# Performance work log

Measured on AMD Instinct MI355X. Metric: run time of the kernel, lower is better.

## Reference

```python
import jax, jax.numpy as jnp
import numpy as np


def _chamfer_sq(points, gts):
    # points: [B,N,3], gts: [B,M,3]
    pn = jnp.sum(points * points, axis=-1)              # [B,N]
    gn = jnp.sum(gts * gts, axis=-1)                    # [B,M]
    cross = jnp.einsum('bnd,bmd->bnm', points, gts)     # [B,N,M]
    d = pn[:, :, None] + gn[:, None, :] - 2.0 * cross   # [B,N,M]
    d = jnp.maximum(d, 0.0)
    p2g = jnp.min(d, axis=2)                            # [B,N] squared NN dist
    g2p = jnp.min(d, axis=1)                            # [B,M]
    return p2g, g2p


def setup_inputs() -> dict:
    key = jax.random.key(0)
    k1, k2 = jax.random.split(key)
    B, N, M = 8, 4096, 4096
    points = jax.random.normal(k1, (B, N, 3), dtype=jnp.float32)
    gts = jax.random.normal(k2, (B, M, 3), dtype=jnp.float32)
    return {"points": points, "gts": gts}


def reference(points, gts):
    p2g_sq, g2p_sq = _chamfer_sq(points, gts)
    p2g = jnp.sqrt(jnp.mean(p2g_sq, axis=1))   # [B]
    g2p = jnp.sqrt(jnp.mean(g2p_sq, axis=1))   # [B]
    loss = (p2g + g2p) / 2.0
    return (jnp.mean(loss), jnp.mean(p2g), jnp.mean(g2p))
```

## Files before the change

### kernel.cpp

```cpp
#include <hip/hip_runtime.h>
#include <math.h>

#define NPTS 4096
#define NB   8
#define QCB  512
#define RCB  512
#define NQC  (NPTS / QCB)
#define NRC  (NPTS / RCB)
#define NRT  (RCB / 32)

typedef _Float16 h8     __attribute__((ext_vector_type(8)));
typedef float    f32x16 __attribute__((ext_vector_type(16)));

__device__ __forceinline__ void split2(float v, _Float16& h, _Float16& l) {
    h = (_Float16)v;
    l = (_Float16)(v - (float)h);
}

__global__ __launch_bounds__(1024, 2) void chamfer_mfma32(
    const float* __restrict__ P, const float* __restrict__ G,
    float* __restrict__ qpart,
    float* __restrict__ rpart,
    int* __restrict__ counter)
{
    __shared__ __align__(16) unsigned char smem[73728];
    h8*    Bfr  = (h8*)smem;
    int*   rbuf = (int*)(smem + 16384);
    float* qbufall = (float*)smem;

    const int b    = blockIdx.y;
    const int qc   = blockIdx.x >> 3;
    const int rc   = blockIdx.x & 7;
    const int tid  = threadIdx.x;
    const int w    = tid >> 6;
    const int lane = tid & 63;
    const int col  = lane & 31;
    const int kg   = lane >> 5;

    if (blockIdx.x == 0 && blockIdx.y == 0 && tid == 0) *counter = 0;

    const float* __restrict__ Pb = P + (size_t)b * NPTS * 3;
    const float* __restrict__ Gb = G + (size_t)b * NPTS * 3;

    const _Float16 one = (_Float16)1.f, zr = (_Float16)0.f;

    if (tid < 512) rbuf[tid] = 0x7f7fffff;
    for (int e = tid; e < NRT * 64; e += 1024) {
        const int el   = e & 63;
        const int ecol = el & 31, ekg = el >> 5;
        const int ref  = rc * RCB + (e >> 6) * 32 + ecol;
        const float gx = Gb[3 * ref], gy = Gb[3 * ref + 1], gz = Gb[3 * ref + 2];
        const float gn = fmaf(gx, gx, fmaf(gy, gy, gz * gz));
        _Float16 xh, xl, yh, yl, zh, zl, nh, nl;
        split2(gx, xh, xl); split2(gy, yh, yl); split2(gz, zh, zl); split2(gn, nh, nl);
        Bfr[e] = ekg ? (h8){one, nh, xl, yl, zl, zr, nl, zr}
                     : (h8){xh, yh, zh, one, nh, xh, yh, zh};
    }

    const int q0 = qc * QCB + w * 32 + col;
    const float px = Pb[3 * q0], py = Pb[3 * q0 + 1], pz = Pb[3 * q0 + 2];
    const float m2x = -2.f * px, m2y = -2.f * py, m2z = -2.f * pz;
    const float pn = fmaf(px, px, fmaf(py, py, pz * pz));
    _Float16 axh, axl, ayh, ayl, azh, azl, aph, apl;
    split2(m2x, axh, axl); split2(m2y, ayh, ayl); split2(m2z, azh, azl); split2(pn, aph, apl);
    const h8 afr = kg ? (h8){apl, zr, axh, ayh, azh, aph, one, zr}
                      : (h8){axh, ayh, azh, aph, one, axl, ayl, azl};

    f32x16 qacc;
#pragma unroll
    for (int j = 0; j < 16; ++j) qacc[j] = 3.4e38f;

    __syncthreads();

    const f32x16 cz = (f32x16){0.f,0.f,0.f,0.f,0.f,0.f,0.f,0.f,
                               0.f,0.f,0.f,0.f,0.f,0.f,0.f,0.f};
#pragma unroll 4
    for (int rt = 0; rt < NRT; ++rt) {
        const h8 bfr = Bfr[rt * 64 + lane];
        f32x16 d = __builtin_amdgcn_mfma_f32_32x32x16_f16(afr, bfr, cz, 0, 0, 0);
#pragma unroll
        for (int j = 0; j < 16; ++j) qacc[j] = fminf(qacc[j], d[j]);
        float t0 = fminf(fminf(d[0],  d[1]),  d[2]);
        float t1 = fminf(fminf(d[3],  d[4]),  d[5]);
        float t2 = fminf(fminf(d[6],  d[7]),  d[8]);
        float t3 = fminf(fminf(d[9],  d[10]), d[11]);
        float t4 = fminf(fminf(d[12], d[13]), d[14]);
        float v  = fminf(fminf(fminf(t0, t1), t2), fminf(fminf(t3, t4), d[15]));
        v = fmaxf(v, 0.f);
        atomicMin(&rbuf[rt * 32 + col], __float_as_int(v));
    }

    __syncthreads();
    if (tid < RCB)
        rpart[((size_t)b * NQC + qc) * NPTS + rc * RCB + tid] = __int_as_float(rbuf[tid]);
    __syncthreads();

    float* qw = qbufall + w * 1152;
#pragma unroll
    for (int j = 0; j < 16; ++j) {
        const int row = (j & 3) + 8 * (j >> 2) + 4 * kg;
        qw[row * 36 + col] = qacc[j];
    }
    __syncthreads();
    if (lane < 32) {
        const float4* qr = (const float4*)(qw + col * 36);
        float4 v = qr[0];
#pragma unroll
        for (int k = 1; k < 8; ++k) {
            float4 u = qr[k];
            v.x = fminf(v.x, u.x); v.y = fminf(v.y, u.y);
            v.z = fminf(v.z, u.z); v.w = fminf(v.w, u.w);
        }
        const float rowmin = fminf(fminf(v.x, v.y), fminf(v.z, v.w));
        qpart[((size_t)b * NRC + rc) * NPTS + qc * QCB + w * 32 + col] = rowmin;
    }
}

__global__ __launch_bounds__(256) void chamfer_reduce2(
    const float* __restrict__ qpart, const float* __restrict__ rpart,
    float* __restrict__ sums, int* __restrict__ counter,
    float* __restrict__ out)
{
    const int path = blockIdx.x >> 5;
    const int b    = (blockIdx.x >> 2) & 7;
    const int sp   = blockIdx.x & 3;
    const float* __restrict__ base = (path ? rpart : qpart) + (size_t)b * 8 * NPTS;

    float sum = 0.f;
#pragma unroll
    for (int i = 0; i < 4; ++i) {
        const int q = sp * 1024 + i * 256 + threadIdx.x;
        float mn = base[q];
#pragma unroll
        for (int c = 1; c < 8; ++c) mn = fminf(mn, base[(size_t)c * NPTS + q]);
        sum += fmaxf(mn, 0.f);
    }

    __shared__ float red[256];
    __shared__ int amLast;
    red[threadIdx.x] = sum;
    __syncthreads();
    if (threadIdx.x < 128) red[threadIdx.x] += red[threadIdx.x + 128];
    __syncthreads();
    if (threadIdx.x < 64) {
        float v = red[threadIdx.x] + red[threadIdx.x + 64];
#pragma unroll
        for (int off = 32; off > 0; off >>= 1) v += __shfl_down(v, off, 64);
        if (threadIdx.x == 0) {
            sums[blockIdx.x] = v;
            __threadfence();
            amLast = (atomicAdd(counter, 1) == 63);
        }
    }
    __syncthreads();

    if (amLast) {
        __shared__ float r16[16];
        if (threadIdx.x < 16) {
            float s = 0.f;
#pragma unroll
            for (int k = 0; k < 4; ++k)
                s += *(volatile const float*)&sums[threadIdx.x * 4 + k];
            r16[threadIdx.x] = sqrtf(s / (float)NPTS);
        }
        __syncthreads();
        if (threadIdx.x == 0) {
            float p2g = 0.f, g2p = 0.f;
#pragma unroll
            for (int bb = 0; bb < NB; ++bb) { p2g += r16[bb]; g2p += r16[NB + bb]; }
            p2g *= (1.0f / NB);
            g2p *= (1.0f / NB);
            out[0] = 0.5f * (p2g + g2p);
            out[1] = p2g;
            out[2] = g2p;
            *counter = 0;
        }
    }
}

extern "C" void kernel_launch(void* const* d_in, const int* in_sizes, int n_in,
                              void* d_out, int out_size, void* d_ws, size_t ws_size,
                              hipStream_t stream) {
    const float* points = (const float*)d_in[0];
    const float* gts    = (const float*)d_in[1];
    float* out = (float*)d_out;

    float* qpart = (float*)d_ws;
    float* rpart = qpart + (size_t)NB * NRC * NPTS;
    float* sums  = rpart + (size_t)NB * NQC * NPTS;
    int*   counter = (int*)(sums + 64);

    dim3 grid1(NQC * NRC, NB);
    chamfer_mfma32<<<grid1, 1024, 0, stream>>>(points, gts, qpart, rpart, counter);

    chamfer_reduce2<<<dim3(64), 256, 0, stream>>>(qpart, rpart, sums, counter, out);
}
```

Measured before the change: 20.51 us.

## Replace per-chunk partial buffers with global atomicMin reductions and an init kernel

The main kernel now folds its per-reference and per-query chunk minima straight into global [B,N] buffers with unsigned atomicMin. This works because the values are clamped to be non-negative, so their float bits order correctly as unsigned integers. The 8-way partial arrays go away, and the final reduce kernel reads only one value per point instead of taking a min over 8 partials. In exchange, a separate init kernel launch is needed to fill the buffers with the max value and reset the counter, and writes become contended global atomics. The change also fully unrolls the reference-tile loop, trims the transpose padding, and drops one block barrier, since each wave only reads its own LDS region.

```diff
diff --git a/kernel.cpp b/kernel.cpp
--- a/kernel.cpp
+++ b/kernel.cpp
@@ -5,9 +5,7 @@
 #define NB   8
 #define QCB  512
 #define RCB  512
-#define NQC  (NPTS / QCB)
-#define NRC  (NPTS / RCB)
-#define NRT  (RCB / 32)
+#define NRT  16
 
 typedef _Float16 h8     __attribute__((ext_vector_type(8)));
 typedef float    f32x16 __attribute__((ext_vector_type(16)));
@@ -17,16 +15,21 @@
     l = (_Float16)(v - (float)h);
 }
 
+__global__ __launch_bounds__(1024) void chamfer_init(unsigned* __restrict__ buf,
+                                                     int* __restrict__ counter) {
+    buf[blockIdx.x * 1024 + threadIdx.x] = 0xFFFFFFFFu;
+    if (blockIdx.x == 0 && threadIdx.x == 0) *counter = 0;
+}
+
 __global__ __launch_bounds__(1024, 2) void chamfer_mfma32(
     const float* __restrict__ P, const float* __restrict__ G,
-    float* __restrict__ qpart,
-    float* __restrict__ rpart,
-    int* __restrict__ counter)
+    unsigned* __restrict__ qmin,
+    unsigned* __restrict__ rmin)
 {
-    __shared__ __align__(16) unsigned char smem[73728];
+    __shared__ __align__(16) unsigned char smem[69632];
     h8*    Bfr  = (h8*)smem;
     int*   rbuf = (int*)(smem + 16384);
-    float* qbufall = (float*)smem;
+    float* qtr  = (float*)smem;
 
     const int b    = blockIdx.y;
     const int qc   = blockIdx.x >> 3;
@@ -37,24 +40,22 @@
     const int col  = lane & 31;
     const int kg   = lane >> 5;
 
-    if (blockIdx.x == 0 && blockIdx.y == 0 && tid == 0) *counter = 0;
-
     const float* __restrict__ Pb = P + (size_t)b * NPTS * 3;
     const float* __restrict__ Gb = G + (size_t)b * NPTS * 3;
 
     const _Float16 one = (_Float16)1.f, zr = (_Float16)0.f;
 
-    if (tid < 512) rbuf[tid] = 0x7f7fffff;
-    for (int e = tid; e < NRT * 64; e += 1024) {
-        const int el   = e & 63;
+    if (tid < RCB) rbuf[tid] = 0x7f7fffff;
+    {
+        const int el   = tid & 63;
         const int ecol = el & 31, ekg = el >> 5;
-        const int ref  = rc * RCB + (e >> 6) * 32 + ecol;
+        const int ref  = rc * RCB + (tid >> 6) * 32 + ecol;
         const float gx = Gb[3 * ref], gy = Gb[3 * ref + 1], gz = Gb[3 * ref + 2];
         const float gn = fmaf(gx, gx, fmaf(gy, gy, gz * gz));
         _Float16 xh, xl, yh, yl, zh, zl, nh, nl;
         split2(gx, xh, xl); split2(gy, yh, yl); split2(gz, zh, zl); split2(gn, nh, nl);
-        Bfr[e] = ekg ? (h8){one, nh, xl, yl, zl, zr, nl, zr}
-                     : (h8){xh, yh, zh, one, nh, xh, yh, zh};
+        Bfr[tid] = ekg ? (h8){one, nh, xl, yl, zl, zr, nl, zr}
+                       : (h8){xh, yh, zh, one, nh, xh, yh, zh};
     }
 
     const int q0 = qc * QCB + w * 32 + col;
@@ -74,7 +75,7 @@
 
     const f32x16 cz = (f32x16){0.f,0.f,0.f,0.f,0.f,0.f,0.f,0.f,
                                0.f,0.f,0.f,0.f,0.f,0.f,0.f,0.f};
-#pragma unroll 4
+#pragma unroll
     for (int rt = 0; rt < NRT; ++rt) {
         const h8 bfr = Bfr[rt * 64 + lane];
         f32x16 d = __builtin_amdgcn_mfma_f32_32x32x16_f16(afr, bfr, cz, 0, 0, 0);
@@ -92,53 +93,45 @@
 
     __syncthreads();
     if (tid < RCB)
-        rpart[((size_t)b * NQC + qc) * NPTS + rc * RCB + tid] = __int_as_float(rbuf[tid]);
+        atomicMin(&rmin[(size_t)b * NPTS + rc * RCB + tid], (unsigned)rbuf[tid]);
     __syncthreads();
 
-    float* qw = qbufall + w * 1152;
+    float* qw = qtr + w * (32 * 34);
 #pragma unroll
     for (int j = 0; j < 16; ++j) {
         const int row = (j & 3) + 8 * (j >> 2) + 4 * kg;
-        qw[row * 36 + col] = qacc[j];
+        qw[row * 34 + col] = qacc[j];
     }
-    __syncthreads();
     if (lane < 32) {
-        const float4* qr = (const float4*)(qw + col * 36);
-        float4 v = qr[0];
+        const float2* qr = (const float2*)(qw + lane * 34);
+        float m = 3.4e38f;
 #pragma unroll
-        for (int k = 1; k < 8; ++k) {
-            float4 u = qr[k];
-            v.x = fminf(v.x, u.x); v.y = fminf(v.y, u.y);
-            v.z = fminf(v.z, u.z); v.w = fminf(v.w, u.w);
+        for (int k = 0; k < 16; ++k) {
+            float2 u = qr[k];
+            m = fminf(m, fminf(u.x, u.y));
         }
-        const float rowmin = fminf(fminf(v.x, v.y), fminf(v.z, v.w));
-        qpart[((size_t)b * NRC + rc) * NPTS + qc * QCB + w * 32 + col] = rowmin;
+        atomicMin(&qmin[(size_t)b * NPTS + qc * QCB + w * 32 + lane],
+                  __float_as_uint(fmaxf(m, 0.f)));
     }
 }
 
 __global__ __launch_bounds__(256) void chamfer_reduce2(
-    const float* __restrict__ qpart, const float* __restrict__ rpart,
-    float* __restrict__ sums, int* __restrict__ counter,
-    float* __restrict__ out)
+    const unsigned* __restrict__ qmin, const unsigned* __restrict__ rmin,
+    float* __restrict__ sums, int* __restrict__ counter, float* __restrict__ out)
 {
-    const int path = blockIdx.x >> 5;
-    const int b    = (blockIdx.x >> 2) & 7;
-    const int sp   = blockIdx.x & 3;
-    const float* __restrict__ base = (path ? rpart : qpart) + (size_t)b * 8 * NPTS;
+    const int t  = blockIdx.x >> 2;
+    const int sp = blockIdx.x & 3;
+    const unsigned* __restrict__ base =
+        (t >= 8) ? rmin + (size_t)(t - 8) * NPTS : qmin + (size_t)t * NPTS;
 
-    float sum = 0.f;
+    float s = 0.f;
 #pragma unroll
-    for (int i = 0; i < 4; ++i) {
-        const int q = sp * 1024 + i * 256 + threadIdx.x;
-        float mn = base[q];
-#pragma unroll
-        for (int c = 1; c < 8; ++c) mn = fminf(mn, base[(size_t)c * NPTS + q]);
-        sum += fmaxf(mn, 0.f);
-    }
+    for (int i = 0; i < 4; ++i)
+        s += __uint_as_float(base[sp * 1024 + i * 256 + threadIdx.x]);
 
     __shared__ float red[256];
     __shared__ int amLast;
-    red[threadIdx.x] = sum;
+    red[threadIdx.x] = s;
     __syncthreads();
     if (threadIdx.x < 128) red[threadIdx.x] += red[threadIdx.x + 128];
     __syncthreads();
@@ -157,11 +150,11 @@
     if (amLast) {
         __shared__ float r16[16];
         if (threadIdx.x < 16) {
-            float s = 0.f;
+            float acc = 0.f;
 #pragma unroll
             for (int k = 0; k < 4; ++k)
-                s += *(volatile const float*)&sums[threadIdx.x * 4 + k];
-            r16[threadIdx.x] = sqrtf(s / (float)NPTS);
+                acc += *(volatile const float*)&sums[threadIdx.x * 4 + k];
+            r16[threadIdx.x] = sqrtf(acc / (float)NPTS);
         }
         __syncthreads();
         if (threadIdx.x == 0) {
@@ -185,13 +178,15 @@
     const float* gts    = (const float*)d_in[1];
     float* out = (float*)d_out;
 
-    float* qpart = (float*)d_ws;
-    float* rpart = qpart + (size_t)NB * NRC * NPTS;
-    float* sums  = rpart + (size_t)NB * NQC * NPTS;
-    int*   counter = (int*)(sums + 64);
+    unsigned* qmin = (unsigned*)d_ws;
+    unsigned* rmin = qmin + (size_t)NB * NPTS;
+    float*    sums = (float*)(rmin + (size_t)NB * NPTS);
+    int*      counter = (int*)(sums + 64);
 
-    dim3 grid1(NQC * NRC, NB);
-    chamfer_mfma32<<<grid1, 1024, 0, stream>>>(points, gts, qpart, rpart, counter);
+    chamfer_init<<<dim3(64), 1024, 0, stream>>>(qmin, counter);
 
-    chamfer_reduce2<<<dim3(64), 256, 0, stream>>>(qpart, rpart, sums, counter, out);
+    dim3 grid1(64, NB);
+    chamfer_mfma32<<<grid1, 1024, 0, stream>>>(points, gts, qmin, rmin);
+
+    chamfer_reduce2<<<dim3(64), 256, 0, stream>>>(qmin, rmin, sums, counter, out);
 }
```

Measured after the change: 23.61 us (median of 2 runs). 15.1% more time.

## Compute both chamfer directions as separate row-min passes instead of LDS atomics

Applied to the files above, without the earlier changes.

The per-tile column minimum via LDS atomicMin is dropped. The pairwise distances are instead computed twice, once per direction (a grid z-dimension swaps points and gts), and only row-min reduction is used. Each wave now holds four query tiles in registers and reuses each B fragment across four MFMAs, with 256-thread blocks over 1024-reference chunks. This removes atomic contention and the LDS column reduction, but doubles the MFMA work and the number of blocks.

```diff
diff --git a/kernel.cpp b/kernel.cpp
--- a/kernel.cpp
+++ b/kernel.cpp
@@ -4,52 +4,54 @@
 #define NPTS 4096
 #define NB   8
 #define QCB  512
-#define RCB  512
+#define RCB  1024
 #define NQC  (NPTS / QCB)
 #define NRC  (NPTS / RCB)
-#define NRT  (RCB / 32)
 
 typedef _Float16 h8     __attribute__((ext_vector_type(8)));
 typedef float    f32x16 __attribute__((ext_vector_type(16)));
+
+#define FOREACH_T(OP) OP(0) OP(1) OP(2) OP(3)
 
 __device__ __forceinline__ void split2(float v, _Float16& h, _Float16& l) {
     h = (_Float16)v;
     l = (_Float16)(v - (float)h);
 }
 
-__global__ __launch_bounds__(1024, 2) void chamfer_mfma32(
+__global__ __launch_bounds__(256, 2) void chamfer_mfma32(
     const float* __restrict__ P, const float* __restrict__ G,
     float* __restrict__ qpart,
     float* __restrict__ rpart,
     int* __restrict__ counter)
 {
-    __shared__ __align__(16) unsigned char smem[73728];
-    h8*    Bfr  = (h8*)smem;
-    int*   rbuf = (int*)(smem + 16384);
-    float* qbufall = (float*)smem;
+    __shared__ __align__(16) unsigned char smem[32768];
+    h8*    Bfr = (h8*)smem;
+    float* qtr = (float*)smem;
 
-    const int b    = blockIdx.y;
-    const int qc   = blockIdx.x >> 3;
-    const int rc   = blockIdx.x & 7;
-    const int tid  = threadIdx.x;
+    const int dir = blockIdx.z;
+    const int b   = blockIdx.y;
+    const int qc  = blockIdx.x >> 2;
+    const int rc  = blockIdx.x & 3;
+    const int tid = threadIdx.x;
     const int w    = tid >> 6;
     const int lane = tid & 63;
     const int col  = lane & 31;
     const int kg   = lane >> 5;
 
-    if (blockIdx.x == 0 && blockIdx.y == 0 && tid == 0) *counter = 0;
+    if (blockIdx.x == 0 && b == 0 && dir == 0 && tid == 0) *counter = 0;
 
-    const float* __restrict__ Pb = P + (size_t)b * NPTS * 3;
-    const float* __restrict__ Gb = G + (size_t)b * NPTS * 3;
+    const float* __restrict__ Qb = (dir ? G : P) + (size_t)b * NPTS * 3;
+    const float* __restrict__ Rb = (dir ? P : G) + (size_t)b * NPTS * 3;
 
     const _Float16 one = (_Float16)1.f, zr = (_Float16)0.f;
 
-    if (tid < 512) rbuf[tid] = 0x7f7fffff;
-    for (int e = tid; e < NRT * 64; e += 1024) {
+#pragma unroll
+    for (int i = 0; i < 8; ++i) {
+        const int e    = tid + i * 256;
         const int el   = e & 63;
         const int ecol = el & 31, ekg = el >> 5;
         const int ref  = rc * RCB + (e >> 6) * 32 + ecol;
-        const float gx = Gb[3 * ref], gy = Gb[3 * ref + 1], gz = Gb[3 * ref + 2];
+        const float gx = Rb[3 * ref], gy = Rb[3 * ref + 1], gz = Rb[3 * ref + 2];
         const float gn = fmaf(gx, gx, fmaf(gy, gy, gz * gz));
         _Float16 xh, xl, yh, yl, zh, zl, nh, nl;
         split2(gx, xh, xl); split2(gy, yh, yl); split2(gz, zh, zl); split2(gn, nh, nl);
@@ -57,74 +59,73 @@
                      : (h8){xh, yh, zh, one, nh, xh, yh, zh};
     }
 
-    const int q0 = qc * QCB + w * 32 + col;
-    const float px = Pb[3 * q0], py = Pb[3 * q0 + 1], pz = Pb[3 * q0 + 2];
-    const float m2x = -2.f * px, m2y = -2.f * py, m2z = -2.f * pz;
-    const float pn = fmaf(px, px, fmaf(py, py, pz * pz));
-    _Float16 axh, axl, ayh, ayl, azh, azl, aph, apl;
-    split2(m2x, axh, axl); split2(m2y, ayh, ayl); split2(m2z, azh, azl); split2(pn, aph, apl);
-    const h8 afr = kg ? (h8){apl, zr, axh, ayh, azh, aph, one, zr}
-                      : (h8){axh, ayh, azh, aph, one, axl, ayl, azl};
-
-    f32x16 qacc;
-#pragma unroll
-    for (int j = 0; j < 16; ++j) qacc[j] = 3.4e38f;
+#define DECLT(t) h8 afr##t; f32x16 qa##t;
+    FOREACH_T(DECLT)
+#undef DECLT
+#define MKA(t) { \
+        const int q0 = qc * QCB + w * 128 + (t) * 32 + col;                   \
+        const float px = Qb[3 * q0], py = Qb[3 * q0 + 1], pz = Qb[3 * q0 + 2];\
+        const float m2x = -2.f * px, m2y = -2.f * py, m2z = -2.f * pz;        \
+        const float pn = fmaf(px, px, fmaf(py, py, pz * pz));                 \
+        _Float16 xh, xl, yh, yl, zh, zl, ph, pl;                              \
+        split2(m2x, xh, xl); split2(m2y, yh, yl); split2(m2z, zh, zl);        \
+        split2(pn, ph, pl);                                                   \
+        afr##t = kg ? (h8){pl, zr, xh, yh, zh, ph, one, zr}                   \
+                    : (h8){xh, yh, zh, ph, one, xl, yl, zl};                  \
+        _Pragma("unroll")                                                     \
+        for (int j = 0; j < 16; ++j) qa##t[j] = 3.4e38f; }
+    FOREACH_T(MKA)
+#undef MKA
 
     __syncthreads();
 
     const f32x16 cz = (f32x16){0.f,0.f,0.f,0.f,0.f,0.f,0.f,0.f,
                                0.f,0.f,0.f,0.f,0.f,0.f,0.f,0.f};
-#pragma unroll 4
-    for (int rt = 0; rt < NRT; ++rt) {
+#pragma unroll 2
+    for (int rt = 0; rt < 32; ++rt) {
         const h8 bfr = Bfr[rt * 64 + lane];
-        f32x16 d = __builtin_amdgcn_mfma_f32_32x32x16_f16(afr, bfr, cz, 0, 0, 0);
-#pragma unroll
-        for (int j = 0; j < 16; ++j) qacc[j] = fminf(qacc[j], d[j]);
-        float t0 = fminf(fminf(d[0],  d[1]),  d[2]);
-        float t1 = fminf(fminf(d[3],  d[4]),  d[5]);
-        float t2 = fminf(fminf(d[6],  d[7]),  d[8]);
-        float t3 = fminf(fminf(d[9],  d[10]), d[11]);
-        float t4 = fminf(fminf(d[12], d[13]), d[14]);
-        float v  = fminf(fminf(fminf(t0, t1), t2), fminf(fminf(t3, t4), d[15]));
-        v = fmaxf(v, 0.f);
-        atomicMin(&rbuf[rt * 32 + col], __float_as_int(v));
+#define DOT(t) { \
+        f32x16 d = __builtin_amdgcn_mfma_f32_32x32x16_f16(afr##t, bfr, cz, 0, 0, 0); \
+        _Pragma("unroll")                                                     \
+        for (int j = 0; j < 16; ++j) qa##t[j] = fminf(qa##t[j], d[j]); }
+        FOREACH_T(DOT)
+#undef DOT
     }
 
     __syncthreads();
-    if (tid < RCB)
-        rpart[((size_t)b * NQC + qc) * NPTS + rc * RCB + tid] = __int_as_float(rbuf[tid]);
-    __syncthreads();
 
-    float* qw = qbufall + w * 1152;
-#pragma unroll
-    for (int j = 0; j < 16; ++j) {
-        const int row = (j & 3) + 8 * (j >> 2) + 4 * kg;
-        qw[row * 36 + col] = qacc[j];
-    }
-    __syncthreads();
-    if (lane < 32) {
-        const float4* qr = (const float4*)(qw + col * 36);
-        float4 v = qr[0];
-#pragma unroll
-        for (int k = 1; k < 8; ++k) {
-            float4 u = qr[k];
-            v.x = fminf(v.x, u.x); v.y = fminf(v.y, u.y);
-            v.z = fminf(v.z, u.z); v.w = fminf(v.w, u.w);
-        }
-        const float rowmin = fminf(fminf(v.x, v.y), fminf(v.z, v.w));
-        qpart[((size_t)b * NRC + rc) * NPTS + qc * QCB + w * 32 + col] = rowmin;
-    }
+    float* qw = qtr + w * 1088;
+    float* outb = (dir ? rpart : qpart)
+                + ((size_t)b * NRC + rc) * NPTS + qc * QCB + w * 128;
+#define EPI(t) { \
+        _Pragma("unroll")                                                     \
+        for (int j = 0; j < 16; ++j) {                                        \
+            const int row = (j & 3) + 8 * (j >> 2) + 4 * kg;                  \
+            qw[row * 34 + col] = qa##t[j];                                    \
+        }                                                                     \
+        if (lane < 32) {                                                      \
+            const float2* qr = (const float2*)(qw + lane * 34);               \
+            float m = 3.4e38f;                                                \
+            _Pragma("unroll")                                                 \
+            for (int k = 0; k < 16; ++k) {                                    \
+                float2 u = qr[k];                                             \
+                m = fminf(m, fminf(u.x, u.y));                                \
+            }                                                                 \
+            outb[(t) * 32 + lane] = fmaxf(m, 0.f);                            \
+        } }
+    FOREACH_T(EPI)
+#undef EPI
 }
 
 __global__ __launch_bounds__(256) void chamfer_reduce2(
     const float* __restrict__ qpart, const float* __restrict__ rpart,
-    float* __restrict__ sums, int* __restrict__ counter,
-    float* __restrict__ out)
+    float* __restrict__ sums, int* __restrict__ counter, float* __restrict__ out)
 {
-    const int path = blockIdx.x >> 5;
-    const int b    = (blockIdx.x >> 2) & 7;
-    const int sp   = blockIdx.x & 3;
-    const float* __restrict__ base = (path ? rpart : qpart) + (size_t)b * 8 * NPTS;
+    const int t  = blockIdx.x >> 2;
+    const int sp = blockIdx.x & 3;
+    const float* __restrict__ base =
+        (t >= 8 ? rpart + (size_t)(t - 8) * NRC * NPTS
+                : qpart + (size_t)t * NRC * NPTS);
 
     float sum = 0.f;
 #pragma unroll
@@ -132,8 +133,8 @@
         const int q = sp * 1024 + i * 256 + threadIdx.x;
         float mn = base[q];
 #pragma unroll
-        for (int c = 1; c < 8; ++c) mn = fminf(mn, base[(size_t)c * NPTS + q]);
-        sum += fmaxf(mn, 0.f);
+        for (int c = 1; c < NRC; ++c) mn = fminf(mn, base[(size_t)c * NPTS + q]);
+        sum += mn;
     }
 
     __shared__ float red[256];
@@ -157,11 +158,11 @@
     if (amLast) {
         __shared__ float r16[16];
         if (threadIdx.x < 16) {
-            float s = 0.f;
+            float acc = 0.f;
 #pragma unroll
             for (int k = 0; k < 4; ++k)
-                s += *(volatile const float*)&sums[threadIdx.x * 4 + k];
-            r16[threadIdx.x] = sqrtf(s / (float)NPTS);
+                acc += *(volatile const float*)&sums[threadIdx.x * 4 + k];
+            r16[threadIdx.x] = sqrtf(acc / (float)NPTS);
         }
         __syncthreads();
         if (threadIdx.x == 0) {
@@ -187,11 +188,11 @@
 
     float* qpart = (float*)d_ws;
     float* rpart = qpart + (size_t)NB * NRC * NPTS;
-    float* sums  = rpart + (size_t)NB * NQC * NPTS;
+    float* sums  = rpart + (size_t)NB * NRC * NPTS;
     int*   counter = (int*)(sums + 64);
 
-    dim3 grid1(NQC * NRC, NB);
-    chamfer_mfma32<<<grid1, 1024, 0, stream>>>(points, gts, qpart, rpart, counter);
+    dim3 grid1(NQC * NRC, NB, 2);
+    chamfer_mfma32<<<grid1, 256, 0, stream>>>(points, gts, qpart, rpart, counter);
 
     chamfer_reduce2<<<dim3(64), 256, 0, stream>>>(qpart, rpart, sums, counter, out);
 }
```

Measured after the change: 22.43 us. 1.09x slower.
